# Kernel optimization log

Measured on AMD Instinct MI355X. Metric: run time of the kernel, lower is better.

Reference implementation:

```python
import jax, jax.numpy as jnp
import numpy as np

N = 100000       # nodes
E = 1600000      # edges (avg degree 16)
F_IN, H, C = 128, 128, 47


def setup_inputs() -> dict:
    key = jax.random.key(0)
    ks = jax.random.split(key, 12)
    def lin(k, fan_in, fan_out):
        return (jax.random.normal(k, (fan_in, fan_out), dtype=jnp.float32)
                / np.float32(np.sqrt(fan_in)))
    return {
        "x": jax.random.normal(ks[0], (N, F_IN), dtype=jnp.float32),
        "src": jax.random.randint(ks[1], (E,), 0, N, dtype=jnp.int32),
        "dst": jax.random.randint(ks[2], (E,), 0, N, dtype=jnp.int32),
        "w_self0": lin(ks[3], F_IN, H),
        "w_neigh0": lin(ks[4], F_IN, H),
        "b0": jnp.zeros((H,), jnp.float32),
        "w_self1": lin(ks[5], H, H),
        "w_neigh1": lin(ks[6], H, H),
        "b1": jnp.zeros((H,), jnp.float32),
        "w_self2": lin(ks[7], H, C),
        "w_neigh2": lin(ks[8], H, C),
        "b2": jnp.zeros((C,), jnp.float32),
    }


def _sage_layer(h, src, dst, w_self, w_neigh, b):
    # mean-aggregate neighbor features: gather h[src], scatter-add to dst
    agg = jax.ops.segment_sum(h[src], dst, num_segments=N)        # [N, d]
    deg = jax.ops.segment_sum(jnp.ones((src.shape[0], 1), h.dtype), dst,
                              num_segments=N)                     # [N, 1]
    mean = agg / jnp.maximum(deg, 1.0)
    # DGL SAGEConv('mean'): fc_self(h_dst) + fc_neigh(mean) + bias
    return h @ w_self + mean @ w_neigh + b


def reference(x, src, dst,
              w_self0, w_neigh0, b0,
              w_self1, w_neigh1, b1,
              w_self2, w_neigh2, b2):
    h = _sage_layer(x, src, dst, w_self0, w_neigh0, b0)
    h = jax.nn.relu(h)  # dropout is identity in eval mode
    h = _sage_layer(h, src, dst, w_self1, w_neigh1, b1)
    h = jax.nn.relu(h)
    h = _sage_layer(h, src, dst, w_self2, w_neigh2, b2)
    return h
```

## Files before the change

### kernel.cpp

```cpp
#include <hip/hip_runtime.h>

typedef unsigned int u32;
typedef unsigned short u16;
typedef __attribute__((ext_vector_type(8))) short short8;
typedef __attribute__((ext_vector_type(4))) float f32x4;

#define POOLCAP 65536
#define IDXMASK 0x1ffff
#define BUCKCAP 12288

__device__ __forceinline__ u16 f2bf(float f) {
    u32 u = __float_as_uint(f);
    u32 r = (u + 0x7fffu + ((u >> 16) & 1u)) >> 16;
    return (u16)r;
}
__device__ __forceinline__ float bf2f(u32 lo16) { return __uint_as_float(lo16 << 16); }

__device__ __forceinline__ void acc_u4p(float2* a, uint4 v) {
    u32 w[4] = {v.x, v.y, v.z, v.w};
#pragma unroll
    for (int i = 0; i < 4; i++) {
        a[i].x += __uint_as_float(w[i] << 16);
        a[i].y += __uint_as_float(w[i] & 0xffff0000u);
    }
}

#define TILE 4096
__global__ __launch_bounds__(512) void scatter_prep(const int* __restrict__ src,
                                                    const int* __restrict__ dst,
                                                    int* __restrict__ cursor,
                                                    uint2* __restrict__ pairs, int E, int NS,
                                                    const float* __restrict__ ws0, const float* __restrict__ wn0, u16* __restrict__ wt0,
                                                    const float* __restrict__ ws1, const float* __restrict__ wn1, u16* __restrict__ wt1,
                                                    const float* __restrict__ ws2, const float* __restrict__ wn2, u16* __restrict__ wt2) {
    if (blockIdx.x >= NS) {
        int local = blockIdx.x - NS;
        const float *ws, *wn;
        u16* wt;
        int dout, HW;
        if (local < 64)       { ws = ws0; wn = wn0; wt = wt0; dout = 128; HW = 128; }
        else if (local < 128) { ws = ws1; wn = wn1; wt = wt1; dout = 128; HW = 128; local -= 64; }
        else                  { ws = ws2; wn = wn2; wt = wt2; dout = 47;  HW = 64;  local -= 128; }
        int idx = local * 512 + threadIdx.x;
        int n = idx >> 7, k = idx & 127;
        float v = 0.f;
        if (n < HW) { if (n < dout) v = ws[k * dout + n]; }
        else { int nn = n - HW; if (nn < dout) v = wn[k * dout + nn]; }
        wt[idx] = f2bf(v);
        return;
    }
    __shared__ int s_cnt[256];
    __shared__ int s_gpos[256];
    const int tid = threadIdx.x;
    const int base = blockIdx.x * TILE;
    const int tn = min(TILE, E - base);
    if (tid < 256) s_cnt[tid] = 0;
    __syncthreads();
    int d[8], s[8], r[8];
#pragma unroll
    for (int j = 0; j < 8; j++) {
        int k = tid + j * 512;
        if (k < tn) {
            d[j] = dst[base + k];
            s[j] = src[base + k];
            r[j] = atomicAdd(&s_cnt[d[j] >> 9], 1);
        } else d[j] = -1;
    }
    __syncthreads();
    if (tid < 256 && s_cnt[tid] > 0) s_gpos[tid] = atomicAdd(&cursor[tid], s_cnt[tid]);
    __syncthreads();
#pragma unroll
    for (int j = 0; j < 8; j++) {
        if (d[j] >= 0) {
            int b = d[j] >> 9;
            int pos = s_gpos[b] + r[j];
            if (pos < BUCKCAP)
                pairs[(size_t)b * BUCKCAP + pos] = make_uint2((u32)d[j], (u32)s[j]);
        }
    }
}

__global__ __launch_bounds__(512) void build_csr3(const uint2* __restrict__ pairs,
                                                  const int* __restrict__ cursor,
                                                  float* __restrict__ invd,
                                                  int* __restrict__ colsF,
                                                  uint2* __restrict__ pool,
                                                  int* __restrict__ gcnt,
                                                  int Nn) {
    __shared__ int s_fix[512 * 32];
    __shared__ int s_cnt[512];
    const int tid = threadIdx.x;
    const int d0 = blockIdx.x * 512;
    const int nd = min(512, Nn - d0);
    const size_t base = (size_t)blockIdx.x * BUCKCAP;
    const int n = min(cursor[blockIdx.x], BUCKCAP);
    s_cnt[tid] = 0;
    __syncthreads();
    for (int k = tid; k < n; k += 512) {
        uint2 pr = pairs[base + k];
        int dl = (int)pr.x - d0;
        int p = atomicAdd(&s_cnt[dl], 1);
        if (p < 32) s_fix[dl * 32 + p] = (int)pr.y;
        else {
            int q = atomicAdd(gcnt, 1);
            if (q < POOLCAP) pool[q] = make_uint2(pr.x, pr.y);
        }
    }
    __syncthreads();
    if (tid < nd) invd[d0 + tid] = 1.0f / (float)max(s_cnt[tid], 1);
    int4* dst4 = (int4*)(colsF + (size_t)d0 * 32);
    for (int k = tid; k < 512 * 32 / 4; k += 512) {
        int node = k >> 3;
        int cnt = s_cnt[node];
        int dg = min(cnt, 0x7fff) << 17;
        int sb = (k & 7) * 4;
        int4 v;
        v.x = ((sb + 0 < cnt) ? s_fix[k * 4 + 0] : Nn) | dg;
        v.y = ((sb + 1 < cnt) ? s_fix[k * 4 + 1] : Nn) | dg;
        v.z = ((sb + 2 < cnt) ? s_fix[k * 4 + 2] : Nn) | dg;
        v.w = ((sb + 3 < cnt) ? s_fix[k * 4 + 3] : Nn) | dg;
        dst4[k] = v;
    }
}

#define KDIM 128
#define KP 136

template <int NCOLS, bool AF32>
__global__ __launch_bounds__(256) void gemm_bf16(const void* __restrict__ Ap,
                                                 const u16* __restrict__ Bt,
                                                 u16* __restrict__ C, int M) {
    __shared__ u16 As[64 * KP];
    __shared__ u16 Bs[128 * KP];
    const int row0 = blockIdx.x * 64;
    const int col0 = blockIdx.y * 128;
    const int tid = threadIdx.x;

#pragma unroll
    for (int i = 0; i < 4; i++) {
        int idx = tid + i * 256;
        int r = idx >> 4, c = idx & 15;
        uint4 v = make_uint4(0, 0, 0, 0);
        if (row0 + r < M) {
            if (AF32) {
                const float* Af = (const float*)Ap;
                const float4* rowp = (const float4*)(Af + (size_t)(row0 + r) * KDIM);
                float4 f0 = rowp[2 * c];
                float4 f1 = rowp[2 * c + 1];
                v.x = (u32)f2bf(f0.x) | ((u32)f2bf(f0.y) << 16);
                v.y = (u32)f2bf(f0.z) | ((u32)f2bf(f0.w) << 16);
                v.z = (u32)f2bf(f1.x) | ((u32)f2bf(f1.y) << 16);
                v.w = (u32)f2bf(f1.z) | ((u32)f2bf(f1.w) << 16);
            } else {
                const u16* Ab = (const u16*)Ap;
                v = ((const uint4*)(Ab + (size_t)(row0 + r) * KDIM))[c];
            }
        }
        ((uint4*)(As + r * KP))[c] = v;
    }
#pragma unroll
    for (int i = 0; i < 8; i++) {
        int idx = tid + i * 256;
        int r = idx >> 4, c = idx & 15;
        uint4 v = ((const uint4*)(Bt + (size_t)(col0 + r) * KDIM))[c];
        ((uint4*)(Bs + r * KP))[c] = v;
    }
    __syncthreads();

    const int lane = tid & 63, wave = tid >> 6;
    const int quad = lane >> 4, l16 = lane & 15;
    const int wcol = wave * 32;

    f32x4 acc[4][2];
#pragma unroll
    for (int mt = 0; mt < 4; mt++)
#pragma unroll
        for (int nt = 0; nt < 2; nt++) acc[mt][nt] = (f32x4){0.f, 0.f, 0.f, 0.f};

#pragma unroll
    for (int kc = 0; kc < 4; kc++) {
        short8 a[4], b[2];
#pragma unroll
        for (int mt = 0; mt < 4; mt++)
            a[mt] = *(const short8*)(As + (size_t)(mt * 16 + l16) * KP + kc * 32 + quad * 8);
#pragma unroll
        for (int nt = 0; nt < 2; nt++)
            b[nt] = *(const short8*)(Bs + (size_t)(wcol + nt * 16 + l16) * KP + kc * 32 + quad * 8);
#pragma unroll
        for (int mt = 0; mt < 4; mt++)
#pragma unroll
            for (int nt = 0; nt < 2; nt++)
                acc[mt][nt] = __builtin_amdgcn_mfma_f32_16x16x32_bf16(a[mt], b[nt], acc[mt][nt], 0, 0, 0);
    }

    __syncthreads();
#pragma unroll
    for (int mt = 0; mt < 4; mt++)
#pragma unroll
        for (int i = 0; i < 4; i++) {
            int rl = mt * 16 + quad * 4 + i;
#pragma unroll
            for (int nt = 0; nt < 2; nt++)
                As[rl * KP + wcol + nt * 16 + l16] = f2bf(acc[mt][nt][i]);
        }
    __syncthreads();
#pragma unroll
    for (int it = 0; it < 4; it++) {
        int idx = tid + it * 256;
        int r = idx >> 4, c8 = idx & 15;
        if (row0 + r <= M)
            *(uint4*)(C + (size_t)(row0 + r) * NCOLS + col0 + c8 * 8) =
                *(const uint4*)(As + r * KP + c8 * 8);
    }
}

template <bool RELU>
__global__ __launch_bounds__(256) void agg128f_k(const u16* __restrict__ out2,
                                                 const int* __restrict__ colsF,
                                                 const float* __restrict__ invd,
                                                 const float* __restrict__ bias,
                                                 const uint2* __restrict__ pool,
                                                 const int* __restrict__ gcnt,
                                                 u16* __restrict__ outp, int Mn) {
    int wave = threadIdx.x >> 6, lane = threadIdx.x & 63;
    int node = blockIdx.x * 4 + wave;
    if (node >= Mn) return;
    int sub = lane >> 4, l16 = lane & 15;
    const u16* tb = out2 + 128 + 8 * l16;
    const int* cp = colsF + node * 32 + sub;
    int s0 = cp[0],  s1 = cp[4],  s2 = cp[8],  s3 = cp[12];
    int s4 = cp[16], s5 = cp[20], s6 = cp[24], s7 = cp[28];
    const int deg = __builtin_amdgcn_readfirstlane(s0 >> 17);
    s0 &= IDXMASK; s1 &= IDXMASK; s2 &= IDXMASK; s3 &= IDXMASK;
    s4 &= IDXMASK; s5 &= IDXMASK; s6 &= IDXMASK; s7 &= IDXMASK;
    float id = invd[node];
    uint4 sv = *(const uint4*)(out2 + (size_t)node * 256 + 8 * l16);
    float4 b0 = *(const float4*)(bias + 8 * l16);
    float4 b1 = *(const float4*)(bias + 8 * l16 + 4);
    uint4 v0 = *(const uint4*)(tb + (size_t)s0 * 256);
    uint4 v1 = *(const uint4*)(tb + (size_t)s1 * 256);
    uint4 v2 = *(const uint4*)(tb + (size_t)s2 * 256);
    uint4 v3 = *(const uint4*)(tb + (size_t)s3 * 256);
    uint4 v4 = *(const uint4*)(tb + (size_t)s4 * 256);
    uint4 v5 = *(const uint4*)(tb + (size_t)s5 * 256);
    uint4 v6 = *(const uint4*)(tb + (size_t)s6 * 256);
    uint4 v7 = *(const uint4*)(tb + (size_t)s7 * 256);
    float2 a[4];
#pragma unroll
    for (int i = 0; i < 4; i++) a[i] = make_float2(0.f, 0.f);
    acc_u4p(a, v0);
    if (deg > 4)  acc_u4p(a, v1);
    if (deg > 8)  acc_u4p(a, v2);
    if (deg > 12) acc_u4p(a, v3);
    if (deg > 16) {
        acc_u4p(a, v4);
        if (deg > 20) acc_u4p(a, v5);
        if (deg > 24) acc_u4p(a, v6);
        if (deg > 28) acc_u4p(a, v7);
    }
    if (deg > 32) {
        int cnt = min(*gcnt, POOLCAP);
        for (int j = 0; j < cnt; j++) {
            uint2 pe = pool[j];
            if ((int)pe.x == node && sub == (j & 3))
                acc_u4p(a, *(const uint4*)(tb + (size_t)pe.y * 256));
        }
    }
    float af[8] = {a[0].x, a[0].y, a[1].x, a[1].y, a[2].x, a[2].y, a[3].x, a[3].y};
#pragma unroll
    for (int j = 0; j < 8; j++) {
        af[j] += __shfl_xor(af[j], 16); af[j] += __shfl_xor(af[j], 32);
    }
    if (sub == 0) {
        float o0 = bf2f(sv.x & 0xffffu) + af[0] * id + b0.x;
        float o1 = bf2f(sv.x >> 16)     + af[1] * id + b0.y;
        float o2 = bf2f(sv.y & 0xffffu) + af[2] * id + b0.z;
        float o3 = bf2f(sv.y >> 16)     + af[3] * id + b0.w;
        float o4 = bf2f(sv.z & 0xffffu) + af[4] * id + b1.x;
        float o5 = bf2f(sv.z >> 16)     + af[5] * id + b1.y;
        float o6 = bf2f(sv.w & 0xffffu) + af[6] * id + b1.z;
        float o7 = bf2f(sv.w >> 16)     + af[7] * id + b1.w;
        if (RELU) {
            o0 = fmaxf(o0, 0.f); o1 = fmaxf(o1, 0.f); o2 = fmaxf(o2, 0.f); o3 = fmaxf(o3, 0.f);
            o4 = fmaxf(o4, 0.f); o5 = fmaxf(o5, 0.f); o6 = fmaxf(o6, 0.f); o7 = fmaxf(o7, 0.f);
        }
        uint4 w;
        w.x = (u32)f2bf(o0) | ((u32)f2bf(o1) << 16);
        w.y = (u32)f2bf(o2) | ((u32)f2bf(o3) << 16);
        w.z = (u32)f2bf(o4) | ((u32)f2bf(o5) << 16);
        w.w = (u32)f2bf(o6) | ((u32)f2bf(o7) << 16);
        *(uint4*)(outp + (size_t)node * 128 + 8 * l16) = w;
    }
}

__global__ __launch_bounds__(256) void agg_out8f_k(const u16* __restrict__ out2,
                                                   const int* __restrict__ colsF,
                                                   const float* __restrict__ invd,
                                                   const float* __restrict__ bias,
                                                   const uint2* __restrict__ pool,
                                                   const int* __restrict__ gcnt,
                                                   float* __restrict__ outp, int Mn) {
    int wave = threadIdx.x >> 6, lane = threadIdx.x & 63;
    int node = blockIdx.x * 4 + wave;
    if (node >= Mn) return;
    int e8 = lane >> 3, l8 = lane & 7;
    const u16* tb = out2 + 64 + 8 * l8;
    const int* cp = colsF + node * 32 + e8;
    int s0 = cp[0], s1 = cp[8], s2 = cp[16], s3 = cp[24];
    const int deg = __builtin_amdgcn_readfirstlane(s0 >> 17);
    s0 &= IDXMASK; s1 &= IDXMASK; s2 &= IDXMASK; s3 &= IDXMASK;
    float id = invd[node];
    uint4 sv = *(const uint4*)(out2 + (size_t)node * 128 + 8 * l8);
    uint4 v0 = *(const uint4*)(tb + (size_t)s0 * 128);
    uint4 v1 = *(const uint4*)(tb + (size_t)s1 * 128);
    uint4 v2 = *(const uint4*)(tb + (size_t)s2 * 128);
    uint4 v3 = *(const uint4*)(tb + (size_t)s3 * 128);
    float2 a[4];
#pragma unroll
    for (int i = 0; i < 4; i++) a[i] = make_float2(0.f, 0.f);
    acc_u4p(a, v0);
    if (deg > 8)  acc_u4p(a, v1);
    if (deg > 16) acc_u4p(a, v2);
    if (deg > 24) acc_u4p(a, v3);
    if (deg > 32) {
        int cnt = min(*gcnt, POOLCAP);
        for (int j = 0; j < cnt; j++) {
            uint2 pe = pool[j];
            if ((int)pe.x == node && e8 == (j & 7))
                acc_u4p(a, *(const uint4*)(tb + (size_t)pe.y * 128));
        }
    }
    float af[8] = {a[0].x, a[0].y, a[1].x, a[1].y, a[2].x, a[2].y, a[3].x, a[3].y};
#pragma unroll
    for (int j = 0; j < 8; j++) {
        af[j] += __shfl_xor(af[j], 8); af[j] += __shfl_xor(af[j], 16); af[j] += __shfl_xor(af[j], 32);
    }
    if (e8 == 0) {
        u32 sw[4] = {sv.x, sv.y, sv.z, sv.w};
        float* orow = outp + (size_t)node * 47;
#pragma unroll
        for (int j = 0; j < 8; j++) {
            int c = 8 * l8 + j;
            if (c < 47) {
                float s = bf2f((j & 1) ? (sw[j >> 1] >> 16) : (sw[j >> 1] & 0xffffu));
                orow[c] = s + af[j] * id + bias[c];
            }
        }
    }
}


extern "C" void kernel_launch(void* const* d_in, const int* in_sizes, int n_in,
                              void* d_out, int out_size, void* d_ws, size_t ws_size,
                              hipStream_t stream) {
    const float* x   = (const float*)d_in[0];
    const int*   src = (const int*)d_in[1];
    const int*   dst = (const int*)d_in[2];
    const float* ws0 = (const float*)d_in[3];
    const float* wn0 = (const float*)d_in[4];
    const float* b0  = (const float*)d_in[5];
    const float* ws1 = (const float*)d_in[6];
    const float* wn1 = (const float*)d_in[7];
    const float* b1  = (const float*)d_in[8];
    const float* ws2 = (const float*)d_in[9];
    const float* wn2 = (const float*)d_in[10];
    const float* b2  = (const float*)d_in[11];

    const int Nn = in_sizes[0] / 128;
    const int E  = in_sizes[1];
    const int nBuckets = (Nn + 511) / 512;
    const int NnPad = nBuckets * 512;
    const int nRowTiles = (Nn + 63) / 64;
    const int NS = (E + TILE - 1) / TILE;

    char* p = (char*)d_ws;
    auto alloc = [&](size_t bytes) -> void* {
        void* r = (void*)p;
        p += (bytes + 255) & ~(size_t)255;
        return r;
    };
    u16*   bufA   = (u16*)alloc((size_t)Nn * 128 * 2);
    u16*   out2   = (u16*)alloc(((size_t)Nn * 256 + 256) * 2);
    u16*   wt0    = (u16*)alloc(256 * 128 * 2);
    u16*   wt1    = (u16*)alloc(256 * 128 * 2);
    u16*   wt2    = (u16*)alloc(128 * 128 * 2);
    float* invd   = (float*)alloc((size_t)Nn * 4);
    int*   colsF  = (int*)alloc((size_t)NnPad * 32 * 4);
    uint2* pool   = (uint2*)alloc((size_t)POOLCAP * 8);
    int*   ctrl   = (int*)alloc(257 * 4);
    int*   cursor = ctrl;
    int*   gcnt   = ctrl + 256;
    uint2* pairs  = (uint2*)bufA;

    hipMemsetAsync(ctrl, 0, 257 * 4, stream);

    scatter_prep<<<NS + 160, 512, 0, stream>>>(src, dst, cursor, pairs, E, NS,
                                               ws0, wn0, wt0, ws1, wn1, wt1, ws2, wn2, wt2);
    build_csr3<<<nBuckets, 512, 0, stream>>>(pairs, cursor, invd, colsF, pool, gcnt, Nn);

    dim3 ggrid(nRowTiles, 2);
    dim3 ggrid1(nRowTiles, 1);
    const int aggGrid = (Nn + 3) / 4;
    gemm_bf16<256, true><<<ggrid, 256, 0, stream>>>(x, wt0, out2, Nn);
    agg128f_k<true><<<aggGrid, 256, 0, stream>>>(out2, colsF, invd, b0, pool, gcnt, bufA, Nn);
    gemm_bf16<256, false><<<ggrid, 256, 0, stream>>>(bufA, wt1, out2, Nn);
    agg128f_k<true><<<aggGrid, 256, 0, stream>>>(out2, colsF, invd, b1, pool, gcnt, bufA, Nn);
    gemm_bf16<128, false><<<ggrid1, 256, 0, stream>>>(bufA, wt2, out2, Nn);
    agg_out8f_k<<<aggGrid, 256, 0, stream>>>(out2, colsF, invd, b2, pool, gcnt, (float*)d_out, Nn);
}
```

Baseline: 373.8 us.

## Fuse edge scatter with layer-0 GEMM and fold ctrl memset into weight prep

The hipMemsetAsync and the weight-conversion blocks move into a small prep kernel that also zeroes the control counters. The edge-scatter blocks and the first-layer x@W GEMM blocks now share one launch, so the two independent phases run concurrently and one launch plus one memset disappear. The scatter path is reworked for 256-thread blocks with 16 edges per thread, and the fused kernel sizes its LDS for the GEMM, which may lower occupancy for the scatter blocks.

```diff
diff --git a/kernel.cpp b/kernel.cpp
--- a/kernel.cpp
+++ b/kernel.cpp
@@ -25,58 +25,152 @@
     }
 }
 
+__global__ __launch_bounds__(512) void prep_ctrl(const float* __restrict__ ws0, const float* __restrict__ wn0, u16* __restrict__ wt0,
+                                                 const float* __restrict__ ws1, const float* __restrict__ wn1, u16* __restrict__ wt1,
+                                                 const float* __restrict__ ws2, const float* __restrict__ wn2, u16* __restrict__ wt2,
+                                                 int* __restrict__ ctrl) {
+    int local = blockIdx.x;
+    if (local >= 160) {
+        if (threadIdx.x < 257) ctrl[threadIdx.x] = 0;
+        return;
+    }
+    const float *ws, *wn;
+    u16* wt;
+    int dout, HW;
+    if (local < 64)       { ws = ws0; wn = wn0; wt = wt0; dout = 128; HW = 128; }
+    else if (local < 128) { ws = ws1; wn = wn1; wt = wt1; dout = 128; HW = 128; local -= 64; }
+    else                  { ws = ws2; wn = wn2; wt = wt2; dout = 47;  HW = 64;  local -= 128; }
+    int idx = local * 512 + threadIdx.x;
+    int n = idx >> 7, k = idx & 127;
+    float v = 0.f;
+    if (n < HW) { if (n < dout) v = ws[k * dout + n]; }
+    else { int nn = n - HW; if (nn < dout) v = wn[k * dout + nn]; }
+    wt[idx] = f2bf(v);
+}
+
 #define TILE 4096
-__global__ __launch_bounds__(512) void scatter_prep(const int* __restrict__ src,
-                                                    const int* __restrict__ dst,
-                                                    int* __restrict__ cursor,
-                                                    uint2* __restrict__ pairs, int E, int NS,
-                                                    const float* __restrict__ ws0, const float* __restrict__ wn0, u16* __restrict__ wt0,
-                                                    const float* __restrict__ ws1, const float* __restrict__ wn1, u16* __restrict__ wt1,
-                                                    const float* __restrict__ ws2, const float* __restrict__ wn2, u16* __restrict__ wt2) {
-    if (blockIdx.x >= NS) {
-        int local = blockIdx.x - NS;
-        const float *ws, *wn;
-        u16* wt;
-        int dout, HW;
-        if (local < 64)       { ws = ws0; wn = wn0; wt = wt0; dout = 128; HW = 128; }
-        else if (local < 128) { ws = ws1; wn = wn1; wt = wt1; dout = 128; HW = 128; local -= 64; }
-        else                  { ws = ws2; wn = wn2; wt = wt2; dout = 47;  HW = 64;  local -= 128; }
-        int idx = local * 512 + threadIdx.x;
-        int n = idx >> 7, k = idx & 127;
-        float v = 0.f;
-        if (n < HW) { if (n < dout) v = ws[k * dout + n]; }
-        else { int nn = n - HW; if (nn < dout) v = wn[k * dout + nn]; }
-        wt[idx] = f2bf(v);
+#define KDIM 128
+#define KP 136
+#define GEMM_LDS (64 * KP * 2 + 128 * KP * 2)
+
+__global__ __launch_bounds__(256) void scatter_gemm0(const int* __restrict__ src,
+                                                     const int* __restrict__ dst,
+                                                     int* __restrict__ cursor,
+                                                     uint2* __restrict__ pairs, int E, int NS,
+                                                     const float* __restrict__ x,
+                                                     const u16* __restrict__ Bt,
+                                                     u16* __restrict__ C,
+                                                     int Nn, int nRowTiles) {
+    __shared__ __align__(16) char lds[GEMM_LDS];
+    const int tid = threadIdx.x;
+
+    if (blockIdx.x < NS) {
+        int* s_cnt  = (int*)lds;
+        int* s_gpos = (int*)(lds + 1024);
+        const int base = blockIdx.x * TILE;
+        const int tn = min(TILE, E - base);
+        s_cnt[tid] = 0;
+        __syncthreads();
+        int d[16], s[16], r[16];
+#pragma unroll
+        for (int j = 0; j < 16; j++) {
+            int k = tid + j * 256;
+            if (k < tn) {
+                d[j] = dst[base + k];
+                s[j] = src[base + k];
+                r[j] = atomicAdd(&s_cnt[d[j] >> 9], 1);
+            } else d[j] = -1;
+        }
+        __syncthreads();
+        if (s_cnt[tid] > 0) s_gpos[tid] = atomicAdd(&cursor[tid], s_cnt[tid]);
+        __syncthreads();
+#pragma unroll
+        for (int j = 0; j < 16; j++) {
+            if (d[j] >= 0) {
+                int b = d[j] >> 9;
+                int pos = s_gpos[b] + r[j];
+                if (pos < BUCKCAP)
+                    pairs[(size_t)b * BUCKCAP + pos] = make_uint2((u32)d[j], (u32)s[j]);
+            }
+        }
         return;
     }
-    __shared__ int s_cnt[256];
-    __shared__ int s_gpos[256];
-    const int tid = threadIdx.x;
-    const int base = blockIdx.x * TILE;
-    const int tn = min(TILE, E - base);
-    if (tid < 256) s_cnt[tid] = 0;
-    __syncthreads();
-    int d[8], s[8], r[8];
-#pragma unroll
-    for (int j = 0; j < 8; j++) {
-        int k = tid + j * 512;
-        if (k < tn) {
-            d[j] = dst[base + k];
-            s[j] = src[base + k];
-            r[j] = atomicAdd(&s_cnt[d[j] >> 9], 1);
-        } else d[j] = -1;
-    }
-    __syncthreads();
-    if (tid < 256 && s_cnt[tid] > 0) s_gpos[tid] = atomicAdd(&cursor[tid], s_cnt[tid]);
-    __syncthreads();
-#pragma unroll
-    for (int j = 0; j < 8; j++) {
-        if (d[j] >= 0) {
-            int b = d[j] >> 9;
-            int pos = s_gpos[b] + r[j];
-            if (pos < BUCKCAP)
-                pairs[(size_t)b * BUCKCAP + pos] = make_uint2((u32)d[j], (u32)s[j]);
-        }
+    u16* As = (u16*)lds;
+    u16* Bs = (u16*)(lds + 64 * KP * 2);
+    const int g = blockIdx.x - NS;
+    const int row0 = (g % nRowTiles) * 64;
+    const int col0 = (g / nRowTiles) * 128;
+    const int M = Nn;
+
+#pragma unroll
+    for (int i = 0; i < 4; i++) {
+        int idx = tid + i * 256;
+        int r = idx >> 4, c = idx & 15;
+        uint4 v = make_uint4(0, 0, 0, 0);
+        if (row0 + r < M) {
+            const float4* rowp = (const float4*)(x + (size_t)(row0 + r) * KDIM);
+            float4 f0 = rowp[2 * c];
+            float4 f1 = rowp[2 * c + 1];
+            v.x = (u32)f2bf(f0.x) | ((u32)f2bf(f0.y) << 16);
+            v.y = (u32)f2bf(f0.z) | ((u32)f2bf(f0.w) << 16);
+            v.z = (u32)f2bf(f1.x) | ((u32)f2bf(f1.y) << 16);
+            v.w = (u32)f2bf(f1.z) | ((u32)f2bf(f1.w) << 16);
+        }
+        ((uint4*)(As + r * KP))[c] = v;
+    }
+#pragma unroll
+    for (int i = 0; i < 8; i++) {
+        int idx = tid + i * 256;
+        int r = idx >> 4, c = idx & 15;
+        uint4 v = ((const uint4*)(Bt + (size_t)(col0 + r) * KDIM))[c];
+        ((uint4*)(Bs + r * KP))[c] = v;
+    }
+    __syncthreads();
+
+    const int lane = tid & 63, wave = tid >> 6;
+    const int quad = lane >> 4, l16 = lane & 15;
+    const int wcol = wave * 32;
+
+    f32x4 acc[4][2];
+#pragma unroll
+    for (int mt = 0; mt < 4; mt++)
+#pragma unroll
+        for (int nt = 0; nt < 2; nt++) acc[mt][nt] = (f32x4){0.f, 0.f, 0.f, 0.f};
+
+#pragma unroll
+    for (int kc = 0; kc < 4; kc++) {
+        short8 a[4], bfr[2];
+#pragma unroll
+        for (int mt = 0; mt < 4; mt++)
+            a[mt] = *(const short8*)(As + (size_t)(mt * 16 + l16) * KP + kc * 32 + quad * 8);
+#pragma unroll
+        for (int nt = 0; nt < 2; nt++)
+            bfr[nt] = *(const short8*)(Bs + (size_t)(wcol + nt * 16 + l16) * KP + kc * 32 + quad * 8);
+#pragma unroll
+        for (int mt = 0; mt < 4; mt++)
+#pragma unroll
+            for (int nt = 0; nt < 2; nt++)
+                acc[mt][nt] = __builtin_amdgcn_mfma_f32_16x16x32_bf16(a[mt], bfr[nt], acc[mt][nt], 0, 0, 0);
+    }
+
+    __syncthreads();
+#pragma unroll
+    for (int mt = 0; mt < 4; mt++)
+#pragma unroll
+        for (int i = 0; i < 4; i++) {
+            int rl = mt * 16 + quad * 4 + i;
+#pragma unroll
+            for (int nt = 0; nt < 2; nt++)
+                As[rl * KP + wcol + nt * 16 + l16] = f2bf(acc[mt][nt][i]);
+        }
+    __syncthreads();
+#pragma unroll
+    for (int it = 0; it < 4; it++) {
+        int idx = tid + it * 256;
+        int r = idx >> 4, c8 = idx & 15;
+        if (row0 + r <= M)
+            *(uint4*)(C + (size_t)(row0 + r) * 256 + col0 + c8 * 8) =
+                *(const uint4*)(As + r * KP + c8 * 8);
     }
 }
 
@@ -122,9 +216,6 @@
         dst4[k] = v;
     }
 }
-
-#define KDIM 128
-#define KP 136
 
 template <int NCOLS, bool AF32>
 __global__ __launch_bounds__(256) void gemm_bf16(const void* __restrict__ Ap,
@@ -392,16 +483,14 @@
     int*   gcnt   = ctrl + 256;
     uint2* pairs  = (uint2*)bufA;
 
-    hipMemsetAsync(ctrl, 0, 257 * 4, stream);
-
-    scatter_prep<<<NS + 160, 512, 0, stream>>>(src, dst, cursor, pairs, E, NS,
-                                               ws0, wn0, wt0, ws1, wn1, wt1, ws2, wn2, wt2);
+    prep_ctrl<<<161, 512, 0, stream>>>(ws0, wn0, wt0, ws1, wn1, wt1, ws2, wn2, wt2, ctrl);
+    scatter_gemm0<<<NS + nRowTiles * 2, 256, 0, stream>>>(src, dst, cursor, pairs, E, NS,
+                                                          x, wt0, out2, Nn, nRowTiles);
     build_csr3<<<nBuckets, 512, 0, stream>>>(pairs, cursor, invd, colsF, pool, gcnt, Nn);
 
     dim3 ggrid(nRowTiles, 2);
     dim3 ggrid1(nRowTiles, 1);
     const int aggGrid = (Nn + 3) / 4;
-    gemm_bf16<256, true><<<ggrid, 256, 0, stream>>>(x, wt0, out2, Nn);
     agg128f_k<true><<<aggGrid, 256, 0, stream>>>(out2, colsF, invd, b0, pool, gcnt, bufA, Nn);
     gemm_bf16<256, false><<<ggrid, 256, 0, stream>>>(bufA, wt1, out2, Nn);
     agg128f_k<true><<<aggGrid, 256, 0, stream>>>(out2, colsF, invd, b1, pool, gcnt, bufA, Nn);
```

Result: no change. 366.9 us (-1.9%).
